# Optimization experiments

Measured on AMD Instinct MI355X. Metric: run time of the kernel, lower is better.

Reference implementation:

```python
import jax, jax.numpy as jnp
import numpy as np
from numpy.polynomial.legendre import leggauss

N_COMP = 16
H = W = 1024
G_CONST = 0.004301
SOFT = 0.0


def setup_inputs() -> dict:
    key = jax.random.key(0)
    kx, ky, kz, ks, ksig, kq = jax.random.split(key, 6)
    x = jax.random.normal(kx, (H, W), dtype=jnp.float32) * 5.0
    y = jax.random.normal(ky, (H, W), dtype=jnp.float32) * 5.0
    z = jax.random.normal(kz, (H, W), dtype=jnp.float32) * 1.0
    surf = jax.random.uniform(ks, (N_COMP,), dtype=jnp.float32, minval=0.1, maxval=10.0)
    sigma = jax.random.uniform(ksig, (N_COMP,), dtype=jnp.float32, minval=0.5, maxval=5.0)
    qobs = jax.random.uniform(kq, (N_COMP,), dtype=jnp.float32, minval=0.6, maxval=0.95)
    M_to_L = jnp.asarray(1.5, dtype=jnp.float32)
    inc = jnp.asarray(1.2, dtype=jnp.float32)  # cos(1.2)~0.362 < min(qobs) -> valid deprojection
    m_bh = jnp.asarray(8.0, dtype=jnp.float32)
    return {"x": x, "y": y, "z": z, "surf": surf, "sigma": sigma, "qobs": qobs,
            "M_to_L": M_to_L, "inc": inc, "m_bh": m_bh, "quad_points": 128}


def reference(x, y, z, surf, sigma, qobs, M_to_L, inc, m_bh, quad_points):
    dtype = x.dtype
    cos_inc = jnp.cos(inc)
    sin_inc = jnp.sin(inc)
    q_intr = jnp.sqrt(qobs ** 2 - cos_inc ** 2) / sin_inc                  # [K]
    sqrt_2pi = np.sqrt(2.0 * np.pi).astype(np.float32)
    mass_density = surf * M_to_L * qobs / (q_intr * sigma * sqrt_2pi)      # [K]

    R_flat = jnp.sqrt(x.ravel() ** 2 + y.ravel() ** 2 + z.ravel() ** 2)    # [N]
    scale = jnp.quantile(sigma, 0.5)
    sigma_sc = sigma / scale
    R_sc = R_flat / scale
    soft_sc = SOFT / scale

    mds = jnp.quantile(sigma_sc, 0.5)
    mxs = jnp.max(sigma_sc)
    t_low = jnp.arcsinh(jnp.log(1e-7 * mds) * 2.0 / jnp.pi)
    t_high = jnp.arcsinh(jnp.log(1000.0 * mxs) * 2.0 / jnp.pi)

    # Gauss-Legendre nodes on [-1,1] (static), mapped to [t_low, t_high] (traced)
    xleg, wleg = leggauss(int(quad_points))
    xleg = jnp.asarray(xleg, dtype=dtype)
    wleg = jnp.asarray(wleg, dtype=dtype)
    half = 0.5 * (t_high - t_low)
    mid = 0.5 * (t_high + t_low)
    t_1d = half * xleg + mid                                               # [Q]
    w_1d = half * wleg                                                     # [Q]

    # double-exponential transform u = exp(pi/2 sinh t)
    u_1d = jnp.exp(jnp.pi / 2.0 * jnp.sinh(t_1d))
    du_1d = jnp.pi / 2.0 * jnp.cosh(t_1d) * u_1d

    R2 = R_sc ** 2                                                          # [N]
    coef_k = q_intr * mass_density                                          # [K]
    inv_sig2 = 1.0 / sigma_sc ** 2                                          # [K]

    # scan over quadrature nodes; each step is an [N,K] tile reduced to [N]
    def body(acc, juw):
        u_j, duw_j = juw
        one_plus = 1.0 + u_j
        e = jnp.exp((-0.5 / one_plus) * R2[:, None] * inv_sig2[None, :])    # [N,K]
        denom_k = one_plus ** 2 * jnp.sqrt(q_intr ** 2 + u_j)               # [K]
        acc = acc + (e @ (coef_k / denom_k)) * duw_j
        return acc, None

    integral, _ = jax.lax.scan(body, jnp.zeros_like(R2), (u_1d, du_1d * w_1d))

    vc2_mge = (2.0 * jnp.pi * G_CONST * scale ** 2) * integral
    vc2_bh = G_CONST * 10.0 ** m_bh / scale * (R2 + soft_sc ** 2) ** (-1.5)
    v_rot_flat = R_sc * jnp.sqrt(vc2_mge + vc2_bh)
    return v_rot_flat.reshape(x.shape)
```

## Files before the change

### kernel.cpp

```cpp
#include <hip/hip_runtime.h>

#define QN 128
#define KN 16
#define TERMS (QN*KN)
#define MBLK 256

#define TBL 2048
#define BBLK 128
#define EPB  (TBL/BBLK)
#define TPE  (256/EPB)

#define TMIN_F (-34.0f)
#define TMAX_F (16.0f)
#define DT_F   ((TMAX_F - TMIN_F) / (float)(TBL - 1))
#define INV_DT_F ((float)(TBL - 1) / (TMAX_F - TMIN_F))
#define TBL_OFF 16

#define G_CONST   0.004301
#define LOG2E_D   1.4426950408889634
#define PI_D      3.141592653589793
#define HALF_PI_D 1.5707963267948966
#define SQRT_2PI_D 2.5066282746310002

__device__ __forceinline__ float exp2_fast(float v) {
#if __has_builtin(__builtin_amdgcn_exp2f)
  return __builtin_amdgcn_exp2f(v);
#else
  return exp2f(v);
#endif
}

__global__ __launch_bounds__(256) void mge_build(
    const float* __restrict__ surf, const float* __restrict__ sigma,
    const float* __restrict__ qobs, const float* __restrict__ M_to_L,
    const float* __restrict__ inc, const float* __restrict__ m_bh,
    float* __restrict__ ws)
{
  __shared__ double s_a[QN + 1], s_b[QN + 1];
  __shared__ double s_node[QN], s_wleg[QN];
  __shared__ double s_scal[3];
  __shared__ double s_coef[KN], s_invsig2[KN], s_qintr2[KN];
  __shared__ float sA[TERMS], sW[TERMS];
  const int t = threadIdx.x;

  if (t < QN) { int j = t + 1; s_a[j] = (2.0 * j - 1.0) / j; s_b[j] = (double)(j - 1) / j; }
  __syncthreads();

  if (t < QN / 2) {
    double z = cos(PI_D * (t + 0.75) / (QN + 0.5));
    double p1 = 0.0, pp = 0.0;
    for (int it = 0; it < 5; ++it) {
      p1 = 1.0; double p2 = 0.0;
      for (int j = 1; j <= QN; ++j) {
        double p3 = p2; p2 = p1;
        p1 = s_a[j] * z * p2 - s_b[j] * p3;
      }
      pp = QN * (z * p1 - p2) / (z * z - 1.0);
      if (it < 4) z -= p1 / pp;
    }
    double w = 2.0 / ((1.0 - z * z) * pp * pp);
    s_node[t] = -z; s_node[QN - 1 - t] = z;
    s_wleg[t] = w;  s_wleg[QN - 1 - t] = w;
  }

  if (t == 192) {
    double cosi = cos((double)inc[0]), sini = sin((double)inc[0]);
    double ML = (double)M_to_L[0];
    float ss[KN];
    for (int k = 0; k < KN; ++k) ss[k] = sigma[k];
    for (int i = 1; i < KN; ++i) {
      float v = ss[i]; int j = i - 1;
      while (j >= 0 && ss[j] > v) { ss[j + 1] = ss[j]; --j; }
      ss[j + 1] = v;
    }
    double scale = 0.5 * ((double)ss[KN/2 - 1] + (double)ss[KN/2]);
    double mds = 0.5 * ((double)ss[KN/2 - 1] / scale + (double)ss[KN/2] / scale);
    double mxs = (double)ss[KN - 1] / scale;
    double t_low  = asinh(log(1e-7 * mds) * 2.0 / PI_D);
    double t_high = asinh(log(1000.0 * mxs) * 2.0 / PI_D);
    s_scal[0] = 0.5 * (t_high - t_low);
    s_scal[1] = 0.5 * (t_high + t_low);
    s_scal[2] = 2.0 * PI_D * G_CONST * scale * scale;
    for (int k = 0; k < KN; ++k) {
      double q = (double)qobs[k], sg = (double)sigma[k];
      double qi = sqrt(q * q - cosi * cosi) / sini;
      double md = (double)surf[k] * ML * q / (qi * sg * SQRT_2PI_D);
      double sgsc = sg / scale;
      s_coef[k] = qi * md;
      s_invsig2[k] = 1.0 / (sgsc * sgsc);
      s_qintr2[k] = qi * qi;
    }
    if (blockIdx.x == 0) {
      ws[0] = (float)(1.0 / (scale * scale));
      ws[1] = (float)(G_CONST * pow(10.0, (double)m_bh[0]) / scale);
    }
  }
  __syncthreads();

  if (t < QN) {
    double half = s_scal[0], mid = s_scal[1], mgec = s_scal[2];
    double tt = half * s_node[t] + mid;
    double sh = sinh(tt), ch = cosh(tt);
    double u  = exp(HALF_PI_D * sh);
    double duw = HALF_PI_D * ch * u * (half * s_wleg[t]);
    double op = 1.0 + u;
    double nh_over = -0.5 / op;
    double inv_op2 = 1.0 / (op * op);
    for (int k = 0; k < KN; ++k) {
      sA[t * KN + k] = (float)(nh_over * s_invsig2[k] * LOG2E_D);
      sW[t * KN + k] = (float)(mgec * duw * s_coef[k] * inv_op2 / sqrt(s_qintr2[k] + u));
    }
  }
  __syncthreads();

  const int e   = t / TPE;
  const int sub = t % TPE;
  const int entry = blockIdx.x * EPB + e;
  const float r2 = exp2_fast(TMIN_F + entry * DT_F);
  float acc = 0.f;
  for (int q = sub; q < TERMS; q += TPE)
    acc += sW[q] * exp2_fast(sA[q] * r2);
#pragma unroll
  for (int off = TPE / 2; off; off >>= 1) acc += __shfl_down(acc, off);
  if (sub == 0) ws[TBL_OFF + entry] = acc;
}

__global__ __launch_bounds__(MBLK) void mge_main(
    const float* __restrict__ x, const float* __restrict__ y,
    const float* __restrict__ z, const float* __restrict__ ws,
    float* __restrict__ out, int n)
{
  __shared__ float sT[TBL];
  const int t = threadIdx.x;
  const float* __restrict__ tbl = ws + TBL_OFF;
  for (int i = t; i < TBL / 4; i += MBLK)
    ((float4*)sT)[i] = ((const float4*)tbl)[i];
  const float inv_scale2 = ws[0];
  const float bh_coef    = ws[1];
  __syncthreads();

  const int g = blockIdx.x * MBLK + t;
  const int base = 4 * g;
  if (base + 3 < n) {
    float4 xv = ((const float4*)x)[g];
    float4 yv = ((const float4*)y)[g];
    float4 zv = ((const float4*)z)[g];
    float r2[4] = {
      (xv.x*xv.x + yv.x*yv.x + zv.x*zv.x) * inv_scale2,
      (xv.y*xv.y + yv.y*yv.y + zv.y*zv.y) * inv_scale2,
      (xv.z*xv.z + yv.z*yv.z + zv.z*zv.z) * inv_scale2,
      (xv.w*xv.w + yv.w*yv.w + zv.w*zv.w) * inv_scale2 };
    float4 ov;
    float* o = &ov.x;
#pragma unroll
    for (int i = 0; i < 4; ++i) {
      float r = r2[i];
      float idxf = (__log2f(r) - TMIN_F) * INV_DT_F;
      idxf = fminf(fmaxf(idxf, 0.0f), (float)(TBL - 1) - 0.001f);
      int ii = (int)idxf;
      float frac = idxf - (float)ii;
      float f0 = sT[ii], f1 = sT[ii + 1];
      float F = f0 + frac * (f1 - f0);
      float rs = rsqrtf(r);
      float vc2 = F + bh_coef * (rs * rs * rs);
      o[i] = sqrtf(r * vc2);
    }
    ((float4*)out)[g] = ov;
  } else {
    for (int p = base; p < n; ++p) {
      float xx = x[p], yy = y[p], zz = z[p];
      float r = (xx*xx + yy*yy + zz*zz) * inv_scale2;
      float idxf = (__log2f(r) - TMIN_F) * INV_DT_F;
      idxf = fminf(fmaxf(idxf, 0.0f), (float)(TBL - 1) - 0.001f);
      int ii = (int)idxf;
      float frac = idxf - (float)ii;
      float f0 = sT[ii], f1 = sT[ii + 1];
      float F = f0 + frac * (f1 - f0);
      float rs = rsqrtf(r);
      float vc2 = F + bh_coef * (rs * rs * rs);
      out[p] = sqrtf(r * vc2);
    }
  }
}

extern "C" void kernel_launch(void* const* d_in, const int* in_sizes, int n_in,
                              void* d_out, int out_size, void* d_ws, size_t ws_size,
                              hipStream_t stream) {
  const float* x      = (const float*)d_in[0];
  const float* y      = (const float*)d_in[1];
  const float* z      = (const float*)d_in[2];
  const float* surf   = (const float*)d_in[3];
  const float* sigma  = (const float*)d_in[4];
  const float* qobs   = (const float*)d_in[5];
  const float* M_to_L = (const float*)d_in[6];
  const float* inc    = (const float*)d_in[7];
  const float* m_bh   = (const float*)d_in[8];

  float* ws  = (float*)d_ws;
  float* out = (float*)d_out;
  const int n = in_sizes[0];

  hipLaunchKernelGGL(mge_build, dim3(BBLK), dim3(256), 0, stream,
                     surf, sigma, qobs, M_to_L, inc, m_bh, ws);
  const int grid = (n / 4 + MBLK - 1) / MBLK;
  hipLaunchKernelGGL(mge_main, dim3(grid), dim3(MBLK), 0, stream,
                     x, y, z, ws, out, n);
}
```

Before: 102.0 us.

## Fuse table build and main evaluation into one cooperative kernel with grid sync

Merges the two kernels into a single cooperative launch: the first 128 blocks build the interpolation table, then a grid-wide sync lets every block load the table and evaluate points. Shared memory is reused through a union of build scratch and the table. It also seeds the Legendre root Newton iteration with a better initial guess and cuts it from 5 to 3 iterations. This removes one kernel launch and its gap, but every block now waits at the grid barrier, and cooperative launch has its own overhead. The grid is clamped to 2048 blocks, and the main loop still indexes by block, so inputs larger than 2048*1024 elements would be left partly unprocessed.

```diff
diff --git a/kernel.cpp b/kernel.cpp
--- a/kernel.cpp
+++ b/kernel.cpp
@@ -1,4 +1,7 @@
 #include <hip/hip_runtime.h>
+#include <hip/hip_cooperative_groups.h>
+
+namespace cg = cooperative_groups;
 
 #define QN 128
 #define KN 16
@@ -30,111 +33,123 @@
 #endif
 }
 
-__global__ __launch_bounds__(256) void mge_build(
+struct BuildScratch {
+  double a[QN + 1], b[QN + 1];
+  double node[QN], wleg[QN];
+  double scal[3];
+  double coef[KN], invsig2[KN], qintr2[KN];
+  float  A[TERMS], W[TERMS];
+};
+
+union SharedU {
+  BuildScratch bld;
+  float tbl[TBL];
+};
+
+__global__ __launch_bounds__(MBLK) void mge_fused(
+    const float* __restrict__ x, const float* __restrict__ y,
+    const float* __restrict__ z,
     const float* __restrict__ surf, const float* __restrict__ sigma,
     const float* __restrict__ qobs, const float* __restrict__ M_to_L,
     const float* __restrict__ inc, const float* __restrict__ m_bh,
-    float* __restrict__ ws)
+    float* __restrict__ ws, float* __restrict__ out, int n)
 {
-  __shared__ double s_a[QN + 1], s_b[QN + 1];
-  __shared__ double s_node[QN], s_wleg[QN];
-  __shared__ double s_scal[3];
-  __shared__ double s_coef[KN], s_invsig2[KN], s_qintr2[KN];
-  __shared__ float sA[TERMS], sW[TERMS];
+  __shared__ SharedU sh;
   const int t = threadIdx.x;
-
-  if (t < QN) { int j = t + 1; s_a[j] = (2.0 * j - 1.0) / j; s_b[j] = (double)(j - 1) / j; }
-  __syncthreads();
-
-  if (t < QN / 2) {
-    double z = cos(PI_D * (t + 0.75) / (QN + 0.5));
-    double p1 = 0.0, pp = 0.0;
-    for (int it = 0; it < 5; ++it) {
-      p1 = 1.0; double p2 = 0.0;
-      for (int j = 1; j <= QN; ++j) {
-        double p3 = p2; p2 = p1;
-        p1 = s_a[j] * z * p2 - s_b[j] * p3;
-      }
-      pp = QN * (z * p1 - p2) / (z * z - 1.0);
-      if (it < 4) z -= p1 / pp;
-    }
-    double w = 2.0 / ((1.0 - z * z) * pp * pp);
-    s_node[t] = -z; s_node[QN - 1 - t] = z;
-    s_wleg[t] = w;  s_wleg[QN - 1 - t] = w;
+  cg::grid_group grid = cg::this_grid();
+
+  if (blockIdx.x < BBLK) {
+    if (t < QN) { int j = t + 1; sh.bld.a[j] = (2.0 * j - 1.0) / j; sh.bld.b[j] = (double)(j - 1) / j; }
+    __syncthreads();
+
+    if (t < QN / 2) {
+      double cs = cos(PI_D * (t + 0.75) / (QN + 0.5));
+      double n2 = (double)QN * (double)QN;
+      double z = cs * (1.0 - 1.0 / (8.0 * n2) + 1.0 / (8.0 * n2 * (double)QN));
+      double p1 = 0.0, pp = 0.0;
+      for (int it = 0; it < 3; ++it) {
+        p1 = 1.0; double p2 = 0.0;
+        for (int j = 1; j <= QN; ++j) {
+          double p3 = p2; p2 = p1;
+          p1 = sh.bld.a[j] * z * p2 - sh.bld.b[j] * p3;
+        }
+        pp = QN * (z * p1 - p2) / (z * z - 1.0);
+        if (it < 2) z -= p1 / pp;
+      }
+      double w = 2.0 / ((1.0 - z * z) * pp * pp);
+      sh.bld.node[t] = -z; sh.bld.node[QN - 1 - t] = z;
+      sh.bld.wleg[t] = w;  sh.bld.wleg[QN - 1 - t] = w;
+    }
+
+    if (t == 192) {
+      double cosi = cos((double)inc[0]), sini = sin((double)inc[0]);
+      double ML = (double)M_to_L[0];
+      float ss[KN];
+      for (int k = 0; k < KN; ++k) ss[k] = sigma[k];
+      for (int i = 1; i < KN; ++i) {
+        float v = ss[i]; int j = i - 1;
+        while (j >= 0 && ss[j] > v) { ss[j + 1] = ss[j]; --j; }
+        ss[j + 1] = v;
+      }
+      double scale = 0.5 * ((double)ss[KN/2 - 1] + (double)ss[KN/2]);
+      double mds = 0.5 * ((double)ss[KN/2 - 1] / scale + (double)ss[KN/2] / scale);
+      double mxs = (double)ss[KN - 1] / scale;
+      double t_low  = asinh(log(1e-7 * mds) * 2.0 / PI_D);
+      double t_high = asinh(log(1000.0 * mxs) * 2.0 / PI_D);
+      sh.bld.scal[0] = 0.5 * (t_high - t_low);
+      sh.bld.scal[1] = 0.5 * (t_high + t_low);
+      sh.bld.scal[2] = 2.0 * PI_D * G_CONST * scale * scale;
+      for (int k = 0; k < KN; ++k) {
+        double q = (double)qobs[k], sg = (double)sigma[k];
+        double qi = sqrt(q * q - cosi * cosi) / sini;
+        double md = (double)surf[k] * ML * q / (qi * sg * SQRT_2PI_D);
+        double sgsc = sg / scale;
+        sh.bld.coef[k] = qi * md;
+        sh.bld.invsig2[k] = 1.0 / (sgsc * sgsc);
+        sh.bld.qintr2[k] = qi * qi;
+      }
+      if (blockIdx.x == 0) {
+        ws[0] = (float)(1.0 / (scale * scale));
+        ws[1] = (float)(G_CONST * pow(10.0, (double)m_bh[0]) / scale);
+      }
+    }
+    __syncthreads();
+
+    if (t < QN) {
+      double half = sh.bld.scal[0], mid = sh.bld.scal[1], mgec = sh.bld.scal[2];
+      double tt = half * sh.bld.node[t] + mid;
+      double s_ = sinh(tt), c_ = cosh(tt);
+      double u  = exp(HALF_PI_D * s_);
+      double duw = HALF_PI_D * c_ * u * (half * sh.bld.wleg[t]);
+      double op = 1.0 + u;
+      double nh_over = -0.5 / op;
+      double inv_op2 = 1.0 / (op * op);
+      for (int k = 0; k < KN; ++k) {
+        sh.bld.A[t * KN + k] = (float)(nh_over * sh.bld.invsig2[k] * LOG2E_D);
+        sh.bld.W[t * KN + k] = (float)(mgec * duw * sh.bld.coef[k] * inv_op2 / sqrt(sh.bld.qintr2[k] + u));
+      }
+    }
+    __syncthreads();
+
+    {
+      const int e   = t / TPE;
+      const int sub = t % TPE;
+      const int entry = blockIdx.x * EPB + e;
+      const float r2 = exp2_fast(TMIN_F + entry * DT_F);
+      float acc = 0.f;
+      for (int q = sub; q < TERMS; q += TPE)
+        acc += sh.bld.W[q] * exp2_fast(sh.bld.A[q] * r2);
+#pragma unroll
+      for (int off = TPE / 2; off; off >>= 1) acc += __shfl_down(acc, off);
+      if (sub == 0) ws[TBL_OFF + entry] = acc;
+    }
+    __threadfence();
   }
 
-  if (t == 192) {
-    double cosi = cos((double)inc[0]), sini = sin((double)inc[0]);
-    double ML = (double)M_to_L[0];
-    float ss[KN];
-    for (int k = 0; k < KN; ++k) ss[k] = sigma[k];
-    for (int i = 1; i < KN; ++i) {
-      float v = ss[i]; int j = i - 1;
-      while (j >= 0 && ss[j] > v) { ss[j + 1] = ss[j]; --j; }
-      ss[j + 1] = v;
-    }
-    double scale = 0.5 * ((double)ss[KN/2 - 1] + (double)ss[KN/2]);
-    double mds = 0.5 * ((double)ss[KN/2 - 1] / scale + (double)ss[KN/2] / scale);
-    double mxs = (double)ss[KN - 1] / scale;
-    double t_low  = asinh(log(1e-7 * mds) * 2.0 / PI_D);
-    double t_high = asinh(log(1000.0 * mxs) * 2.0 / PI_D);
-    s_scal[0] = 0.5 * (t_high - t_low);
-    s_scal[1] = 0.5 * (t_high + t_low);
-    s_scal[2] = 2.0 * PI_D * G_CONST * scale * scale;
-    for (int k = 0; k < KN; ++k) {
-      double q = (double)qobs[k], sg = (double)sigma[k];
-      double qi = sqrt(q * q - cosi * cosi) / sini;
-      double md = (double)surf[k] * ML * q / (qi * sg * SQRT_2PI_D);
-      double sgsc = sg / scale;
-      s_coef[k] = qi * md;
-      s_invsig2[k] = 1.0 / (sgsc * sgsc);
-      s_qintr2[k] = qi * qi;
-    }
-    if (blockIdx.x == 0) {
-      ws[0] = (float)(1.0 / (scale * scale));
-      ws[1] = (float)(G_CONST * pow(10.0, (double)m_bh[0]) / scale);
-    }
-  }
-  __syncthreads();
-
-  if (t < QN) {
-    double half = s_scal[0], mid = s_scal[1], mgec = s_scal[2];
-    double tt = half * s_node[t] + mid;
-    double sh = sinh(tt), ch = cosh(tt);
-    double u  = exp(HALF_PI_D * sh);
-    double duw = HALF_PI_D * ch * u * (half * s_wleg[t]);
-    double op = 1.0 + u;
-    double nh_over = -0.5 / op;
-    double inv_op2 = 1.0 / (op * op);
-    for (int k = 0; k < KN; ++k) {
-      sA[t * KN + k] = (float)(nh_over * s_invsig2[k] * LOG2E_D);
-      sW[t * KN + k] = (float)(mgec * duw * s_coef[k] * inv_op2 / sqrt(s_qintr2[k] + u));
-    }
-  }
-  __syncthreads();
-
-  const int e   = t / TPE;
-  const int sub = t % TPE;
-  const int entry = blockIdx.x * EPB + e;
-  const float r2 = exp2_fast(TMIN_F + entry * DT_F);
-  float acc = 0.f;
-  for (int q = sub; q < TERMS; q += TPE)
-    acc += sW[q] * exp2_fast(sA[q] * r2);
-#pragma unroll
-  for (int off = TPE / 2; off; off >>= 1) acc += __shfl_down(acc, off);
-  if (sub == 0) ws[TBL_OFF + entry] = acc;
-}
-
-__global__ __launch_bounds__(MBLK) void mge_main(
-    const float* __restrict__ x, const float* __restrict__ y,
-    const float* __restrict__ z, const float* __restrict__ ws,
-    float* __restrict__ out, int n)
-{
-  __shared__ float sT[TBL];
-  const int t = threadIdx.x;
-  const float* __restrict__ tbl = ws + TBL_OFF;
+  grid.sync();
+
   for (int i = t; i < TBL / 4; i += MBLK)
-    ((float4*)sT)[i] = ((const float4*)tbl)[i];
+    ((float4*)sh.tbl)[i] = ((const float4*)(ws + TBL_OFF))[i];
   const float inv_scale2 = ws[0];
   const float bh_coef    = ws[1];
   __syncthreads();
@@ -159,7 +174,7 @@
       idxf = fminf(fmaxf(idxf, 0.0f), (float)(TBL - 1) - 0.001f);
       int ii = (int)idxf;
       float frac = idxf - (float)ii;
-      float f0 = sT[ii], f1 = sT[ii + 1];
+      float f0 = sh.tbl[ii], f1 = sh.tbl[ii + 1];
       float F = f0 + frac * (f1 - f0);
       float rs = rsqrtf(r);
       float vc2 = F + bh_coef * (rs * rs * rs);
@@ -174,7 +189,7 @@
       idxf = fminf(fmaxf(idxf, 0.0f), (float)(TBL - 1) - 0.001f);
       int ii = (int)idxf;
       float frac = idxf - (float)ii;
-      float f0 = sT[ii], f1 = sT[ii + 1];
+      float f0 = sh.tbl[ii], f1 = sh.tbl[ii + 1];
       float F = f0 + frac * (f1 - f0);
       float rs = rsqrtf(r);
       float vc2 = F + bh_coef * (rs * rs * rs);
@@ -198,11 +213,15 @@
 
   float* ws  = (float*)d_ws;
   float* out = (float*)d_out;
-  const int n = in_sizes[0];
-
-  hipLaunchKernelGGL(mge_build, dim3(BBLK), dim3(256), 0, stream,
-                     surf, sigma, qobs, M_to_L, inc, m_bh, ws);
-  const int grid = (n / 4 + MBLK - 1) / MBLK;
-  hipLaunchKernelGGL(mge_main, dim3(grid), dim3(MBLK), 0, stream,
-                     x, y, z, ws, out, n);
+  int n = in_sizes[0];
+
+  int grid = (n / 4 + MBLK - 1) / MBLK;
+  if (grid < BBLK) grid = BBLK;
+  if (grid > 2048) grid = 2048;
+
+  void* args[] = { (void*)&x, (void*)&y, (void*)&z, (void*)&surf, (void*)&sigma,
+                   (void*)&qobs, (void*)&M_to_L, (void*)&inc, (void*)&m_bh,
+                   (void*)&ws, (void*)&out, (void*)&n };
+  hipLaunchCooperativeKernel((const void*)mge_fused, dim3(grid), dim3(MBLK),
+                             args, 0, stream);
 }
```

Result: slower. 167.6 us (+64.3%).
